# Kernel tuning notes

Hardware: AMD Instinct MI355X
Metric: run time of the kernel (lower is better)

## Reference

```python
import jax, jax.numpy as jnp
import numpy as np
from jax import lax

RADIUS = 0.2
MAX_SAMPLES = 64
B, C, N = 16, 3, 2048


def setup_inputs() -> dict:
    key = jax.random.key(0)
    # point clouds uniform in unit cube, layout (B, 3, N) as in pointnet repos
    pcs = jax.random.uniform(key, (B, C, N), dtype=jnp.float32)
    return {"pcs": pcs}


def reference(pcs):
    # Self ball-point query: for every point i, gather up to MAX_SAMPLES indices j
    # with ||p_i - p_j||^2 < RADIUS^2 (in ascending index order, the standard CUDA
    # ball-query scan order); unused slots are padded with the first found index.
    # The query point itself (dist 0) is always within radius, so every row has
    # at least one valid neighbor.
    x = jnp.swapaxes(pcs, 1, 2)                    # (B, N, 3)
    d2 = jnp.sum((x[:, :, None, :] - x[:, None, :, :]) ** 2, axis=-1)  # (B, N, N)
    within = d2 < (RADIUS * RADIUS)
    n = x.shape[1]
    idx = jnp.arange(n, dtype=jnp.int32)
    # key = j if within radius else n (sentinel); smallest K keys = first K neighbors
    keys = jnp.where(within, idx[None, None, :], n)  # (B, N, N) int32
    # top_k of negated keys -> K smallest keys, ascending after negation
    neg_topk, _ = lax.top_k(-keys, MAX_SAMPLES)      # (B, N, K)
    first_k = -neg_topk                              # ascending indices, sentinels last
    first = first_k[..., :1]                         # first valid neighbor (pad value)
    group_idx = jnp.where(first_k == n, first, first_k)
    return group_idx.astype(jnp.int64)
```

## Files before the change

### kernel.cpp

```cpp
#include <hip/hip_runtime.h>
#include <hip/hip_bf16.h>
#include <stdint.h>


#define B_DIM 16
#define N_PTS 2048
#define K_OUT 64
#define R2 0.04f
#define WAVES 8
#define BLOCK_T (WAVES * 64)
#define JPW (N_PTS / WAVES)
#define WPW (JPW / 32)
#define ROWPAD 65

typedef float v2f __attribute__((ext_vector_type(2)));

__global__ __launch_bounds__(BLOCK_T, 8) void ball_query_kernel(
    const float* __restrict__ pcs,
    int* __restrict__ out)
{
#pragma clang fp contract(off)
    __shared__ int rows[64 * ROWPAD];
    __shared__ int cntS[WAVES][64];
    __shared__ int qfS[WAVES][64];

    const int b    = blockIdx.x >> 5;
    const int qg   = blockIdx.x & 31;
    const int tid  = threadIdx.x;
    const int wave = __builtin_amdgcn_readfirstlane(tid >> 6);
    const int lane = tid & 63;

    const float* __restrict__ sx = pcs + (size_t)b * 3 * N_PTS;
    const float* __restrict__ sy = sx + N_PTS;
    const float* __restrict__ sz = sy + N_PTS;

    const int qi = qg * 64 + lane;
    const float qx = sx[qi];
    const float qy = sy[qi];
    const float qz = sz[qi];
    const v2f qx2 = {qx, qx}, qy2 = {qy, qy}, qz2 = {qz, qz};

    const int jbase = wave * JPW;

    unsigned mask[WPW];
    for (int t = 0; t < WPW; ++t) {
        unsigned m = 0;
        #pragma unroll
        for (int k = 30; k >= 0; k -= 2) {
            const int j = jbase + t * 32 + k;
            const v2f px = *(const v2f*)(sx + j);
            const v2f py = *(const v2f*)(sy + j);
            const v2f pz = *(const v2f*)(sz + j);
            const v2f dx = px - qx2;
            const v2f dy = py - qy2;
            const v2f dz = pz - qz2;
            const v2f d2 = (dx * dx + dy * dy) + dz * dz;
            m = m + m + (unsigned)(d2.y < R2);
            m = m + m + (unsigned)(d2.x < R2);
        }
        mask[t] = m;
    }

    int cnt = 0;
    #pragma unroll
    for (int t = 0; t < WPW; ++t) cnt += __builtin_popcount(mask[t]);
    int qf = -1;
    #pragma unroll
    for (int t = 0; t < WPW; ++t) {
        if (qf < 0 && mask[t] != 0u)
            qf = jbase + t * 32 + __builtin_ctz(mask[t]);
    }
    cntS[wave][lane] = cnt;
    qfS[wave][lane]  = qf;
    __syncthreads();

    int base = 0, tc = 0, gfirst = 0;
    #pragma unroll
    for (int w = 0; w < WAVES; ++w) {
        const int c = cntS[w][lane];
        const int f = qfS[w][lane];
        if (w < wave) base += c;
        gfirst = (tc == 0 && c > 0) ? f : gfirst;
        tc += c;
    }

    int slot = base;
    for (int t = 0; t < WPW; ++t) {
        unsigned m = mask[t];
        while (m != 0u && slot < K_OUT) {
            const int k = (int)__builtin_ctz(m);
            rows[lane * ROWPAD + slot] = jbase + t * 32 + k;
            m &= m - 1u;
            ++slot;
        }
    }

    #pragma unroll
    for (int s0 = 0; s0 < K_OUT / WAVES; ++s0) {
        const int s = wave * (K_OUT / WAVES) + s0;
        if (s >= tc) rows[lane * ROWPAD + s] = gfirst;
    }
    __syncthreads();

    int* const obase = out + (size_t)(b * N_PTS + qg * 64) * K_OUT;
    #pragma unroll
    for (int it = 0; it < (64 * K_OUT) / BLOCK_T; ++it) {
        const int idx = it * BLOCK_T + tid;
        const int r = idx >> 6;
        const int c = idx & 63;
        obase[idx] = rows[r * ROWPAD + c];
    }
}

extern "C" void kernel_launch(void* const* d_in, const int* in_sizes, int n_in,
                              void* d_out, int out_size, void* d_ws, size_t ws_size,
                              hipStream_t stream) {
    const float* pcs = (const float*)d_in[0];
    int* out = (int*)d_out;
    const int grid = B_DIM * 32;
    ball_query_kernel<<<grid, BLOCK_T, 0, stream>>>(pcs, out);
}
```

Before: 76.13 us.

## Split ball query into mask-computation and emit kernels via output buffer

Splits the single fused kernel into two launches. The first computes per-query 32-bit neighbor masks over 128-point windows using 2048 blocks of 256 threads, and stores them in the output buffer as scratch. The second reads each query group's masks back, does the prefix count and compaction, and overwrites the same region with indices. The aim is more parallelism in the distance phase, since the old kernel had only 512 blocks. The cost is a second launch plus a global round trip of the mask data.

```diff
diff --git a/kernel.cpp b/kernel.cpp
--- a/kernel.cpp
+++ b/kernel.cpp
@@ -7,47 +7,41 @@
 #define N_PTS 2048
 #define K_OUT 64
 #define R2 0.04f
-#define WAVES 8
-#define BLOCK_T (WAVES * 64)
-#define JPW (N_PTS / WAVES)
-#define WPW (JPW / 32)
 #define ROWPAD 65
 
 typedef float v2f __attribute__((ext_vector_type(2)));
 
-__global__ __launch_bounds__(BLOCK_T, 8) void ball_query_kernel(
+__global__ __launch_bounds__(256, 8) void bq_mask_kernel(
     const float* __restrict__ pcs,
     int* __restrict__ out)
 {
 #pragma clang fp contract(off)
-    __shared__ int rows[64 * ROWPAD];
-    __shared__ int cntS[WAVES][64];
-    __shared__ int qfS[WAVES][64];
-
-    const int b    = blockIdx.x >> 5;
-    const int qg   = blockIdx.x & 31;
+    const int bid  = blockIdx.x;
+    const int qg   = bid >> 2;
+    const int b    = qg >> 5;
+    const int g    = qg & 31;
     const int tid  = threadIdx.x;
     const int wave = __builtin_amdgcn_readfirstlane(tid >> 6);
     const int lane = tid & 63;
+    const int win  = (bid & 3) * 4 + wave;
 
     const float* __restrict__ sx = pcs + (size_t)b * 3 * N_PTS;
     const float* __restrict__ sy = sx + N_PTS;
     const float* __restrict__ sz = sy + N_PTS;
 
-    const int qi = qg * 64 + lane;
-    const float qx = sx[qi];
-    const float qy = sy[qi];
-    const float qz = sz[qi];
+    const int qi = g * 64 + lane;
+    const float qx = sx[qi], qy = sy[qi], qz = sz[qi];
     const v2f qx2 = {qx, qx}, qy2 = {qy, qy}, qz2 = {qz, qz};
 
-    const int jbase = wave * JPW;
+    const int jbase = win * 128;
+    int* const mbase = out + (size_t)qg * 4096;
 
-    unsigned mask[WPW];
-    for (int t = 0; t < WPW; ++t) {
+    #pragma unroll
+    for (int i = 0; i < 4; ++i) {
         unsigned m = 0;
         #pragma unroll
         for (int k = 30; k >= 0; k -= 2) {
-            const int j = jbase + t * 32 + k;
+            const int j = jbase + i * 32 + k;
             const v2f px = *(const v2f*)(sx + j);
             const v2f py = *(const v2f*)(sy + j);
             const v2f pz = *(const v2f*)(sz + j);
@@ -58,17 +52,38 @@
             m = m + m + (unsigned)(d2.y < R2);
             m = m + m + (unsigned)(d2.x < R2);
         }
-        mask[t] = m;
+        mbase[(win * 4 + i) * 64 + lane] = (int)m;
     }
+}
+
+#define WAVES 8
+__global__ __launch_bounds__(512, 4) void bq_emit_kernel(
+    int* __restrict__ out)
+{
+    __shared__ int rows[64 * ROWPAD];
+    __shared__ int cntS[WAVES][64];
+    __shared__ int qfS[WAVES][64];
+
+    const int qg   = blockIdx.x;
+    const int tid  = threadIdx.x;
+    const int wave = tid >> 6;
+    const int lane = tid & 63;
+
+    int* const reg = out + (size_t)qg * 4096;
+
+    unsigned mask[8];
+    #pragma unroll
+    for (int i = 0; i < 8; ++i)
+        mask[i] = (unsigned)reg[(wave * 8 + i) * 64 + lane];
 
     int cnt = 0;
     #pragma unroll
-    for (int t = 0; t < WPW; ++t) cnt += __builtin_popcount(mask[t]);
+    for (int i = 0; i < 8; ++i) cnt += __builtin_popcount(mask[i]);
     int qf = -1;
     #pragma unroll
-    for (int t = 0; t < WPW; ++t) {
-        if (qf < 0 && mask[t] != 0u)
-            qf = jbase + t * 32 + __builtin_ctz(mask[t]);
+    for (int i = 0; i < 8; ++i) {
+        if (qf < 0 && mask[i] != 0u)
+            qf = (wave * 8 + i) * 32 + __builtin_ctz(mask[i]);
     }
     cntS[wave][lane] = cnt;
     qfS[wave][lane]  = qf;
@@ -85,11 +100,12 @@
     }
 
     int slot = base;
-    for (int t = 0; t < WPW; ++t) {
-        unsigned m = mask[t];
+    #pragma unroll
+    for (int i = 0; i < 8; ++i) {
+        unsigned m = mask[i];
         while (m != 0u && slot < K_OUT) {
             const int k = (int)__builtin_ctz(m);
-            rows[lane * ROWPAD + slot] = jbase + t * 32 + k;
+            rows[lane * ROWPAD + slot] = (wave * 8 + i) * 32 + k;
             m &= m - 1u;
             ++slot;
         }
@@ -102,13 +118,12 @@
     }
     __syncthreads();
 
-    int* const obase = out + (size_t)(b * N_PTS + qg * 64) * K_OUT;
     #pragma unroll
-    for (int it = 0; it < (64 * K_OUT) / BLOCK_T; ++it) {
-        const int idx = it * BLOCK_T + tid;
+    for (int it = 0; it < (64 * K_OUT) / 512; ++it) {
+        const int idx = it * 512 + tid;
         const int r = idx >> 6;
         const int c = idx & 63;
-        obase[idx] = rows[r * ROWPAD + c];
+        reg[idx] = rows[r * ROWPAD + c];
     }
 }
 
@@ -117,6 +132,6 @@
                               hipStream_t stream) {
     const float* pcs = (const float*)d_in[0];
     int* out = (int*)d_out;
-    const int grid = B_DIM * 32;
-    ball_query_kernel<<<grid, BLOCK_T, 0, stream>>>(pcs, out);
+    bq_mask_kernel<<<2048, 256, 0, stream>>>(pcs, out);
+    bq_emit_kernel<<<512, 512, 0, stream>>>(out);
 }
```

Result: slower. 77.85 us (+2.3%).
